# Optimization experiments

Hardware: AMD Instinct MI355X
Metric: run time of the kernel (lower is better)

Reference implementation:

```python
import jax, jax.numpy as jnp
import numpy as np

N_ATOMS = 10000
N_EDGES = 500000
N_RADIAL = 5
N_BASIS = 7
N_SPECIES = 119
R_MIN = 0.5
R_MAX = 6.0
N_CONTR = 8
EMB_NORM = 1.0 / np.sqrt(N_BASIS)


def tril_2d_indices(n):
    return np.array([(i, j) for i in range(n) for j in range(i + 1)], dtype=np.int32)


def tril_3d_indices(n):
    return np.array([(i, j, k) for i in range(n) for j in range(i + 1) for k in range(j + 1)], dtype=np.int32)


TRI2 = tril_2d_indices(N_RADIAL)
TRI3 = tril_3d_indices(N_RADIAL)


def setup_inputs() -> dict:
    key = jax.random.key(0)
    k1, k2, k3, k4 = jax.random.split(key, 4)
    dr_vec = jax.random.normal(k1, (N_EDGES, 3), dtype=jnp.float32) * 1.5
    Z = jax.random.randint(k2, (N_ATOMS,), 0, N_SPECIES)
    neighbor_idxs = jax.random.randint(k3, (2, N_EDGES), 0, N_ATOMS)
    embeddings = jax.random.normal(k4, (N_SPECIES, N_SPECIES, N_RADIAL, N_BASIS), dtype=jnp.float32)
    return {"dr_vec": dr_vec, "Z": Z, "neighbor_idxs": neighbor_idxs, "embeddings": embeddings}


def _descriptor(dr_vec, embeddings, Z, neighbor_idxs):
    idx_i, idx_j = neighbor_idxs[0], neighbor_idxs[1]
    dr = jnp.linalg.norm(dr_vec, axis=-1)                      # [E]
    dn = dr_vec / (dr + 1e-5)[:, None]                         # [E,3] unit directions
    # --- radial function: Gaussian basis + species-pair coefficients + cosine cutoff ---
    betta = N_BASIS ** 2 / R_MAX ** 2
    rad_norm = (2.0 * betta / np.pi) ** 0.75
    shifts = (R_MIN + (R_MAX - R_MIN) / N_BASIS * np.arange(N_BASIS)).astype(np.float32)
    basis = rad_norm * jnp.exp(-betta * (dr[:, None] - shifts) ** 2)   # [E,B]
    coeffs = embeddings[Z[idx_i], Z[idx_j]]                            # [E,R,B] gather
    radial = jnp.einsum("erb,eb->er", coeffs, basis) * EMB_NORM        # [E,R]
    cutoff = 0.5 * (jnp.cos(np.pi * jnp.minimum(dr, R_MAX) / R_MAX) + 1.0)
    radial = radial * cutoff[:, None]
    # --- geometric moments: outer products of dn, scatter-added per atom ---
    xyz = dn[:, None, :]                                 # [E,1,3]
    m0 = radial                                          # [E,R]
    m1 = radial[..., None] * xyz                         # [E,R,3]
    m2 = m1[..., None] * xyz[:, :, None, :]              # [E,R,3,3]
    m3 = m2[..., None] * xyz[:, :, None, None, :]        # [E,R,3,3,3]
    seg = lambda x: jax.ops.segment_sum(x, idx_j, num_segments=N_ATOMS)
    M0, M1, M2, M3 = seg(m0), seg(m1), seg(m2), seg(m3)
    # --- triangular moment contractions into invariants ---
    c0 = M0
    c1 = jnp.einsum("ari,asi->ars", M1, M1)
    c2 = jnp.einsum("arij,asij->ars", M2, M2)
    c3 = jnp.einsum("arijk,asijk->ars", M3, M3)
    c4 = jnp.einsum("arij,asik,atjk->arst", M2, M2, M2)
    c5 = jnp.einsum("ari,asj,atij->arst", M1, M1, M2)
    c6 = jnp.einsum("arijk,asijl,atkl->arst", M3, M3, M2)
    c7 = jnp.einsum("arijk,asij,atk->arst", M3, M2, M1)
    i2, j2 = TRI2[:, 0], TRI2[:, 1]
    i3, j3, k3 = TRI3[:, 0], TRI3[:, 1], TRI3[:, 2]
    n_atoms = c0.shape[0]
    c1 = c1[:, i2, j2]
    c2 = c2[:, i2, j2]
    c3 = c3[:, i2, j2]
    c4 = c4[:, i3, j3, k3]
    c5 = c5[:, i2, j2].reshape(n_atoms, -1)   # symmetric in (r,s)
    c6 = c6[:, i2, j2].reshape(n_atoms, -1)   # symmetric in (r,s)
    c7 = c7.reshape(n_atoms, -1)              # no symmetry
    feats = [c0, c1, c2, c3, c4, c5, c6, c7][:N_CONTR]
    return jnp.concatenate(feats, axis=-1)    # [n_atoms, 360]


def reference(dr_vec, Z, neighbor_idxs, embeddings):
    return _descriptor(dr_vec, embeddings, Z, neighbor_idxs)
```

## Files before the change

### kernel.cpp

```cpp
#include <hip/hip_runtime.h>
#include <hip/hip_fp16.h>
#include <cmath>

#define NSPEC 119
#define FEAT 360
#define CAP 128
#define G 16
#define NPAIR (NSPEC*NSPEC*35)
#define CNTSTRIDE 16

__global__ __launch_bounds__(256) void gm_prep_kernel(
    const float* __restrict__ emb, __half* __restrict__ emb_h,
    const int* __restrict__ Z, unsigned char* __restrict__ Zb,
    int* __restrict__ cnt, int n_atoms)
{
    int t = blockIdx.x * 256 + threadIdx.x;
    if (t < NPAIR) {
        int p = t / 35;
        int b = t - p * 35;
        emb_h[(p << 6) + b] = __float2half_rn(emb[t]);
    }
    if (t < n_atoms) {
        Zb[t] = (unsigned char)Z[t];
        cnt[t * CNTSTRIDE] = 0;
    }
}

__global__ __launch_bounds__(256) void gm_scatter_kernel(
    const float* __restrict__ dr_vec,
    const unsigned char* __restrict__ Zb,
    const int* __restrict__ nbr,
    const __half* __restrict__ emb_h,
    int* __restrict__ cnt,
    uint4* __restrict__ bucket,
    int n_edges, float rad_norm)
{
    int t = blockIdx.x * 256 + threadIdx.x;
    int h = (n_edges + 1) >> 1;
    if (t >= h) return;
    int e0 = t;
    int e1 = t + h;
    bool v1 = (e1 < n_edges);
    int e1c = v1 ? e1 : e0;

    int ai0 = nbr[e0],            aj0 = nbr[n_edges + e0];
    int ai1 = nbr[e1c],           aj1 = nbr[n_edges + e1c];

    int pos0 = atomicAdd(&cnt[aj0 * CNTSTRIDE], 1);
    int pos1 = v1 ? atomicAdd(&cnt[aj1 * CNTSTRIDE], 1) : 0;

    float x0 = dr_vec[3*e0+0], y0 = dr_vec[3*e0+1], z0 = dr_vec[3*e0+2];
    float x1 = dr_vec[3*e1c+0], y1 = dr_vec[3*e1c+1], z1 = dr_vec[3*e1c+2];
    int Zi0 = Zb[ai0], Zj0 = Zb[aj0];
    int Zi1 = Zb[ai1], Zj1 = Zb[aj1];

    const uint4* p40 = (const uint4*)(emb_h + ((size_t)(Zi0*NSPEC + Zj0) << 6));
    const uint4* p41 = (const uint4*)(emb_h + ((size_t)(Zi1*NSPEC + Zj1) << 6));
    uint buf0[20], buf1[20];
#pragma unroll
    for (int q = 0; q < 5; ++q) *(uint4*)(buf0 + 4*q) = p40[q];
#pragma unroll
    for (int q = 0; q < 5; ++q) *(uint4*)(buf1 + 4*q) = p41[q];

    const float betta = 49.0f/36.0f;

#pragma unroll
    for (int k = 0; k < 2; ++k) {
        float x = k ? x1 : x0, y = k ? y1 : y0, z = k ? z1 : z0;
        const uint* buf = k ? buf1 : buf0;
        int aj = k ? aj1 : aj0;
        int pos = k ? pos1 : pos0;
        if (k && !v1) break;

        float dr = sqrtf(x*x + y*y + z*z);
        float inv = 1.0f / (dr + 1e-5f);
        float dx = x*inv, dy = y*inv, dz = z*inv;

        float basis[7];
#pragma unroll
        for (int b = 0; b < 7; ++b) {
            float tt = dr - (0.5f + (5.5f/7.0f)*(float)b);
            basis[b] = rad_norm * __expf(-betta*tt*tt);
        }
        float cutoff = 0.5f * (__cosf(fminf(dr, 6.0f) * 0.52359877559829887f) + 1.0f);
        float sc = cutoff * 0.37796447300922720f;

        const __half2* hb = (const __half2*)buf;
        float co[36];
#pragma unroll
        for (int q = 0; q < 18; ++q) {
            float2 f = __half22float2(hb[q]);
            co[2*q]   = f.x;
            co[2*q+1] = f.y;
        }

        float rad[5];
#pragma unroll
        for (int r = 0; r < 5; ++r) {
            float acc = 0.0f;
#pragma unroll
            for (int b = 0; b < 7; ++b) acc = fmaf(co[r*7+b], basis[b], acc);
            rad[r] = acc * sc;
        }

        if (pos < CAP) {
            uint4 rec;
            __half2* rp = (__half2*)&rec;
            rp[0] = __float22half2_rn(make_float2(rad[0], rad[1]));
            rp[1] = __float22half2_rn(make_float2(rad[2], rad[3]));
            rp[2] = __float22half2_rn(make_float2(rad[4], dx));
            rp[3] = __float22half2_rn(make_float2(dy, dz));
            bucket[(size_t)aj * CAP + pos] = rec;
        }
    }
}

__global__ __launch_bounds__(256) void gm_accum_kernel(
    const int* __restrict__ cnt,
    const uint4* __restrict__ bucket,
    float* __restrict__ out,
    int n_atoms)
{
    __shared__ float MS[16][100];
    int tid = blockIdx.x * 256 + threadIdx.x;
    int a  = tid / G;
    int sl = tid & (G-1);
    int la = threadIdx.x >> 4;
    if (a >= n_atoms) return;

    int c = cnt[a * CNTSTRIDE]; if (c > CAP) c = CAP;

    float m[100];
#pragma unroll
    for (int i = 0; i < 100; ++i) m[i] = 0.f;

    for (int k = sl; k < c; k += G) {
        uint4 rec = bucket[(size_t)a * CAP + k];
        const __half2* rp = (const __half2*)&rec;
        float2 f0 = __half22float2(rp[0]);
        float2 f1 = __half22float2(rp[1]);
        float2 f2 = __half22float2(rp[2]);
        float2 f3 = __half22float2(rp[3]);
        float rad[5] = {f0.x, f0.y, f1.x, f1.y, f2.x};
        float dx = f2.y, dy = f3.x, dz = f3.y;

        float p2[6] = {dx*dx, dx*dy, dx*dz, dy*dy, dy*dz, dz*dz};
        float p3[10] = {p2[0]*dx, p2[0]*dy, p2[0]*dz,
                        p2[3]*dx, p2[4]*dx, p2[5]*dx,
                        p2[3]*dy, p2[3]*dz,
                        p2[4]*dz, p2[5]*dz};

#pragma unroll
        for (int r = 0; r < 5; ++r) {
            float v = rad[r];
            m[r] += v;
            m[5 + r*3 + 0] = fmaf(v, dx, m[5 + r*3 + 0]);
            m[5 + r*3 + 1] = fmaf(v, dy, m[5 + r*3 + 1]);
            m[5 + r*3 + 2] = fmaf(v, dz, m[5 + r*3 + 2]);
#pragma unroll
            for (int u = 0; u < 6; ++u)
                m[20 + r*6 + u] = fmaf(v, p2[u], m[20 + r*6 + u]);
#pragma unroll
            for (int u = 0; u < 10; ++u)
                m[50 + r*10 + u] = fmaf(v, p3[u], m[50 + r*10 + u]);
        }
    }

#pragma unroll
    for (int i = 0; i < 100; ++i) {
        m[i] += __shfl_xor(m[i], 1, 64);
        m[i] += __shfl_xor(m[i], 2, 64);
        m[i] += __shfl_xor(m[i], 4, 64);
        m[i] += __shfl_xor(m[i], 8, 64);
    }

    if (sl == 0) {
#pragma unroll
        for (int i = 0; i < 100; ++i) MS[la][i] = m[i];
    }

    float* F = out + (size_t)a * FEAT;
    const float* S = &MS[la][0];

    const int S2[3][3] = {{0,1,2},{1,3,4},{2,4,5}};
    const int S3[3][3][3] = {
        {{0,1,2},{1,3,4},{2,4,5}},
        {{1,3,4},{3,6,7},{4,7,8}},
        {{2,4,5},{4,7,8},{5,8,9}}};
    const float w6[6]   = {1,2,2,1,2,1};
    const float w10[10] = {1,3,3,3,6,3,1,3,3,1};
    const int   PI[6] = {0,0,0,1,1,2};
    const int   PJ[6] = {0,1,2,1,2,2};
    const float PW[6] = {1,2,2,1,2,1};

    if (sl < 5) F[sl] = S[sl];

    int p = sl;
    if (p < 15) {
        int r = (p >= 10) ? 4 : ((p >= 6) ? 3 : ((p >= 3) ? 2 : ((p >= 1) ? 1 : 0)));
        int s = p - (r*(r+1))/2;
        const float* M1r = S + 5  + 3*r;
        const float* M1s = S + 5  + 3*s;
        const float* M2r = S + 20 + 6*r;
        const float* M2s = S + 20 + 6*s;
        const float* M3r = S + 50 + 10*r;
        const float* M3s = S + 50 + 10*s;
        float m1r[3], m1s[3], m2r[6], m2s[6], m3r[10], m3s[10];
#pragma unroll
        for (int i = 0; i < 3; ++i)  { m1r[i] = M1r[i]; m1s[i] = M1s[i]; }
#pragma unroll
        for (int u = 0; u < 6; ++u)  { m2r[u] = M2r[u]; m2s[u] = M2s[u]; }
#pragma unroll
        for (int u = 0; u < 10; ++u) { m3r[u] = M3r[u]; m3s[u] = M3s[u]; }

        float a1 = 0.f, a2 = 0.f, a3 = 0.f;
#pragma unroll
        for (int i = 0; i < 3; ++i)  a1 = fmaf(m1r[i], m1s[i], a1);
#pragma unroll
        for (int u = 0; u < 6; ++u)  a2 = fmaf(w6[u]*m2r[u],  m2s[u], a2);
#pragma unroll
        for (int u = 0; u < 10; ++u) a3 = fmaf(w10[u]*m3r[u], m3s[u], a3);
        F[5 + p]  = a1;
        F[20 + p] = a2;
        F[35 + p] = a3;

        float P[3][3];
#pragma unroll
        for (int j = 0; j < 3; ++j)
#pragma unroll
        for (int k = 0; k < 3; ++k) {
            float acc = 0.f;
#pragma unroll
            for (int i = 0; i < 3; ++i)
                acc = fmaf(m2r[S2[i][j]], m2s[S2[i][k]], acc);
            P[j][k] = acc;
        }
        float PA[6] = {P[0][0], P[0][1]+P[1][0], P[0][2]+P[2][0],
                       P[1][1], P[1][2]+P[2][1], P[2][2]};
        int qb = (r*(r+1)*(r+2))/6 + (s*(s+1))/2;
        for (int t = 0; t <= s; ++t) {
            const float* M2t = S + 20 + 6*t;
            float acc = 0.f;
#pragma unroll
            for (int u = 0; u < 6; ++u) acc = fmaf(PA[u], M2t[u], acc);
            F[50 + qb + t] = acc;
        }

        float A[6] = {m1r[0]*m1s[0],
                      m1r[0]*m1s[1] + m1r[1]*m1s[0],
                      m1r[0]*m1s[2] + m1r[2]*m1s[0],
                      m1r[1]*m1s[1],
                      m1r[1]*m1s[2] + m1r[2]*m1s[1],
                      m1r[2]*m1s[2]};
#pragma unroll
        for (int t = 0; t < 5; ++t) {
            const float* M2t = S + 20 + 6*t;
            float acc = 0.f;
#pragma unroll
            for (int u = 0; u < 6; ++u) acc = fmaf(A[u], M2t[u], acc);
            F[85 + p*5 + t] = acc;
        }

        float Q[3][3];
#pragma unroll
        for (int k = 0; k < 3; ++k)
#pragma unroll
        for (int l = 0; l < 3; ++l) {
            float acc = 0.f;
#pragma unroll
            for (int u = 0; u < 6; ++u)
                acc = fmaf(PW[u]*m3r[S3[PI[u]][PJ[u]][k]],
                           m3s[S3[PI[u]][PJ[u]][l]], acc);
            Q[k][l] = acc;
        }
        float QA[6] = {Q[0][0], Q[0][1]+Q[1][0], Q[0][2]+Q[2][0],
                       Q[1][1], Q[1][2]+Q[2][1], Q[2][2]};
#pragma unroll
        for (int t = 0; t < 5; ++t) {
            const float* M2t = S + 20 + 6*t;
            float acc = 0.f;
#pragma unroll
            for (int u = 0; u < 6; ++u) acc = fmaf(QA[u], M2t[u], acc);
            F[160 + p*5 + t] = acc;
        }
    }

#pragma unroll
    for (int hh = 0; hh < 2; ++hh) {
        int h = sl + 16*hh;
        if (h < 25) {
            int r = h / 5;
            int s = h - 5*r;
            const float* M3r = S + 50 + 10*r;
            const float* M2s = S + 20 + 6*s;
            float m3r[10], m2s[6];
#pragma unroll
            for (int u = 0; u < 10; ++u) m3r[u] = M3r[u];
#pragma unroll
            for (int u = 0; u < 6; ++u)  m2s[u] = M2s[u];
            float B[3];
#pragma unroll
            for (int k = 0; k < 3; ++k) {
                float acc = 0.f;
#pragma unroll
                for (int u = 0; u < 6; ++u)
                    acc = fmaf(PW[u]*m3r[S3[PI[u]][PJ[u]][k]], m2s[u], acc);
                B[k] = acc;
            }
#pragma unroll
            for (int t = 0; t < 5; ++t) {
                const float* M1t = S + 5 + 3*t;
                F[235 + r*25 + s*5 + t] =
                    fmaf(B[0], M1t[0], fmaf(B[1], M1t[1], B[2]*M1t[2]));
            }
        }
    }
}

extern "C" void kernel_launch(void* const* d_in, const int* in_sizes, int n_in,
                              void* d_out, int out_size, void* d_ws, size_t ws_size,
                              hipStream_t stream) {
    const float* dr_vec = (const float*)d_in[0];
    const int*   Z      = (const int*)d_in[1];
    const int*   nbr    = (const int*)d_in[2];
    const float* emb    = (const float*)d_in[3];
    float* out = (float*)d_out;

    int n_edges = in_sizes[0] / 3;
    int n_atoms = in_sizes[1];

    int*           cnt   = (int*)d_ws;
    unsigned char* Zb    = (unsigned char*)((char*)d_ws + 655360);
    __half*        emb_h = (__half*)((char*)d_ws + 665600);
    uint4*         bucket= (uint4*)((char*)d_ws + 2478208);

    float rad_norm = (float)pow(2.0 * (49.0/36.0) / M_PI, 0.75);

    int prep_n = (NPAIR > n_atoms) ? NPAIR : n_atoms;
    gm_prep_kernel<<<(prep_n + 255)/256, 256, 0, stream>>>(emb, emb_h, Z, Zb, cnt, n_atoms);

    int h = (n_edges + 1) / 2;
    gm_scatter_kernel<<<(h + 255)/256, 256, 0, stream>>>(
        dr_vec, Zb, nbr, emb_h, cnt, bucket, n_edges, rad_norm);

    int accum_threads = n_atoms * G;
    gm_accum_kernel<<<(accum_threads + 255)/256, 256, 0, stream>>>(
        cnt, bucket, out, n_atoms);
}
```

Before: 121.8 us.

## Fuse scatter and accumulate kernels into persistent kernel with grid barrier

Merges the edge scatter and per-atom accumulate/contraction kernels into one persistent kernel of 512 blocks that grid-strides over edges, synchronises through a global atomic spin barrier, then grid-strides over atoms. The aim is to remove one kernel launch and the gap between the two stages. In exchange it relies on all 512 blocks being co-resident, uses fewer threads for the edge phase, and has a bounded spin that could silently break out on timeout.

Measured after the change: 212.8 us. +74.7%, slower.

```diff
diff --git a/kernel.cpp b/kernel.cpp
--- a/kernel.cpp
+++ b/kernel.cpp
@@ -8,13 +8,16 @@
 #define G 16
 #define NPAIR (NSPEC*NSPEC*35)
 #define CNTSTRIDE 16
+#define NBLK 512
+#define NTHR 256
 
 __global__ __launch_bounds__(256) void gm_prep_kernel(
     const float* __restrict__ emb, __half* __restrict__ emb_h,
     const int* __restrict__ Z, unsigned char* __restrict__ Zb,
-    int* __restrict__ cnt, int n_atoms)
+    int* __restrict__ cnt, int* __restrict__ bar, int n_atoms)
 {
     int t = blockIdx.x * 256 + threadIdx.x;
+    if (t == 0) *bar = 0;
     if (t < NPAIR) {
         int p = t / 35;
         int b = t - p * 35;
@@ -26,161 +29,116 @@
     }
 }
 
-__global__ __launch_bounds__(256) void gm_scatter_kernel(
+__global__ __launch_bounds__(NTHR, 2) void gm_main(
     const float* __restrict__ dr_vec,
     const unsigned char* __restrict__ Zb,
     const int* __restrict__ nbr,
     const __half* __restrict__ emb_h,
     int* __restrict__ cnt,
     uint4* __restrict__ bucket,
-    int n_edges, float rad_norm)
-{
-    int t = blockIdx.x * 256 + threadIdx.x;
-    int h = (n_edges + 1) >> 1;
-    if (t >= h) return;
-    int e0 = t;
-    int e1 = t + h;
-    bool v1 = (e1 < n_edges);
-    int e1c = v1 ? e1 : e0;
-
-    int ai0 = nbr[e0],            aj0 = nbr[n_edges + e0];
-    int ai1 = nbr[e1c],           aj1 = nbr[n_edges + e1c];
-
-    int pos0 = atomicAdd(&cnt[aj0 * CNTSTRIDE], 1);
-    int pos1 = v1 ? atomicAdd(&cnt[aj1 * CNTSTRIDE], 1) : 0;
-
-    float x0 = dr_vec[3*e0+0], y0 = dr_vec[3*e0+1], z0 = dr_vec[3*e0+2];
-    float x1 = dr_vec[3*e1c+0], y1 = dr_vec[3*e1c+1], z1 = dr_vec[3*e1c+2];
-    int Zi0 = Zb[ai0], Zj0 = Zb[aj0];
-    int Zi1 = Zb[ai1], Zj1 = Zb[aj1];
-
-    const uint4* p40 = (const uint4*)(emb_h + ((size_t)(Zi0*NSPEC + Zj0) << 6));
-    const uint4* p41 = (const uint4*)(emb_h + ((size_t)(Zi1*NSPEC + Zj1) << 6));
-    uint buf0[20], buf1[20];
-#pragma unroll
-    for (int q = 0; q < 5; ++q) *(uint4*)(buf0 + 4*q) = p40[q];
-#pragma unroll
-    for (int q = 0; q < 5; ++q) *(uint4*)(buf1 + 4*q) = p41[q];
-
-    const float betta = 49.0f/36.0f;
-
-#pragma unroll
-    for (int k = 0; k < 2; ++k) {
-        float x = k ? x1 : x0, y = k ? y1 : y0, z = k ? z1 : z0;
-        const uint* buf = k ? buf1 : buf0;
-        int aj = k ? aj1 : aj0;
-        int pos = k ? pos1 : pos0;
-        if (k && !v1) break;
-
-        float dr = sqrtf(x*x + y*y + z*z);
-        float inv = 1.0f / (dr + 1e-5f);
-        float dx = x*inv, dy = y*inv, dz = z*inv;
-
-        float basis[7];
-#pragma unroll
-        for (int b = 0; b < 7; ++b) {
-            float tt = dr - (0.5f + (5.5f/7.0f)*(float)b);
-            basis[b] = rad_norm * __expf(-betta*tt*tt);
-        }
-        float cutoff = 0.5f * (__cosf(fminf(dr, 6.0f) * 0.52359877559829887f) + 1.0f);
-        float sc = cutoff * 0.37796447300922720f;
-
-        const __half2* hb = (const __half2*)buf;
-        float co[36];
-#pragma unroll
-        for (int q = 0; q < 18; ++q) {
-            float2 f = __half22float2(hb[q]);
-            co[2*q]   = f.x;
-            co[2*q+1] = f.y;
-        }
-
-        float rad[5];
-#pragma unroll
-        for (int r = 0; r < 5; ++r) {
-            float acc = 0.0f;
-#pragma unroll
-            for (int b = 0; b < 7; ++b) acc = fmaf(co[r*7+b], basis[b], acc);
-            rad[r] = acc * sc;
-        }
-
-        if (pos < CAP) {
-            uint4 rec;
-            __half2* rp = (__half2*)&rec;
-            rp[0] = __float22half2_rn(make_float2(rad[0], rad[1]));
-            rp[1] = __float22half2_rn(make_float2(rad[2], rad[3]));
-            rp[2] = __float22half2_rn(make_float2(rad[4], dx));
-            rp[3] = __float22half2_rn(make_float2(dy, dz));
-            bucket[(size_t)aj * CAP + pos] = rec;
-        }
-    }
-}
-
-__global__ __launch_bounds__(256) void gm_accum_kernel(
-    const int* __restrict__ cnt,
-    const uint4* __restrict__ bucket,
+    int* __restrict__ bar,
     float* __restrict__ out,
-    int n_atoms)
+    int n_edges, int n_atoms, float rad_norm)
 {
     __shared__ float MS[16][100];
-    int tid = blockIdx.x * 256 + threadIdx.x;
-    int a  = tid / G;
-    int sl = tid & (G-1);
-    int la = threadIdx.x >> 4;
-    if (a >= n_atoms) return;
-
-    int c = cnt[a * CNTSTRIDE]; if (c > CAP) c = CAP;
-
-    float m[100];
-#pragma unroll
-    for (int i = 0; i < 100; ++i) m[i] = 0.f;
-
-    for (int k = sl; k < c; k += G) {
-        uint4 rec = bucket[(size_t)a * CAP + k];
-        const __half2* rp = (const __half2*)&rec;
-        float2 f0 = __half22float2(rp[0]);
-        float2 f1 = __half22float2(rp[1]);
-        float2 f2 = __half22float2(rp[2]);
-        float2 f3 = __half22float2(rp[3]);
-        float rad[5] = {f0.x, f0.y, f1.x, f1.y, f2.x};
-        float dx = f2.y, dy = f3.x, dz = f3.y;
-
-        float p2[6] = {dx*dx, dx*dy, dx*dz, dy*dy, dy*dz, dz*dz};
-        float p3[10] = {p2[0]*dx, p2[0]*dy, p2[0]*dz,
-                        p2[3]*dx, p2[4]*dx, p2[5]*dx,
-                        p2[3]*dy, p2[3]*dz,
-                        p2[4]*dz, p2[5]*dz};
-
-#pragma unroll
-        for (int r = 0; r < 5; ++r) {
-            float v = rad[r];
-            m[r] += v;
-            m[5 + r*3 + 0] = fmaf(v, dx, m[5 + r*3 + 0]);
-            m[5 + r*3 + 1] = fmaf(v, dy, m[5 + r*3 + 1]);
-            m[5 + r*3 + 2] = fmaf(v, dz, m[5 + r*3 + 2]);
-#pragma unroll
-            for (int u = 0; u < 6; ++u)
-                m[20 + r*6 + u] = fmaf(v, p2[u], m[20 + r*6 + u]);
-#pragma unroll
-            for (int u = 0; u < 10; ++u)
-                m[50 + r*10 + u] = fmaf(v, p3[u], m[50 + r*10 + u]);
-        }
-    }
-
-#pragma unroll
-    for (int i = 0; i < 100; ++i) {
-        m[i] += __shfl_xor(m[i], 1, 64);
-        m[i] += __shfl_xor(m[i], 2, 64);
-        m[i] += __shfl_xor(m[i], 4, 64);
-        m[i] += __shfl_xor(m[i], 8, 64);
-    }
-
-    if (sl == 0) {
-#pragma unroll
-        for (int i = 0; i < 100; ++i) MS[la][i] = m[i];
-    }
-
-    float* F = out + (size_t)a * FEAT;
-    const float* S = &MS[la][0];
+    const int tid0 = blockIdx.x * NTHR + threadIdx.x;
+    const int nth  = NBLK * NTHR;
+
+    const float betta = 49.0f/36.0f;
+    int h = (n_edges + 1) >> 1;
+    for (int t = tid0; t < h; t += nth) {
+        int e0 = t;
+        int e1 = t + h;
+        bool v1 = (e1 < n_edges);
+        int e1c = v1 ? e1 : e0;
+
+        int ai0 = nbr[e0],  aj0 = nbr[n_edges + e0];
+        int ai1 = nbr[e1c], aj1 = nbr[n_edges + e1c];
+
+        int pos0 = atomicAdd(&cnt[aj0 * CNTSTRIDE], 1);
+        int pos1 = v1 ? atomicAdd(&cnt[aj1 * CNTSTRIDE], 1) : 0;
+
+        float x0 = dr_vec[3*e0+0],  y0 = dr_vec[3*e0+1],  z0 = dr_vec[3*e0+2];
+        float x1 = dr_vec[3*e1c+0], y1 = dr_vec[3*e1c+1], z1 = dr_vec[3*e1c+2];
+        int Zi0 = Zb[ai0], Zj0 = Zb[aj0];
+        int Zi1 = Zb[ai1], Zj1 = Zb[aj1];
+
+        const uint4* p40 = (const uint4*)(emb_h + ((size_t)(Zi0*NSPEC + Zj0) << 6));
+        const uint4* p41 = (const uint4*)(emb_h + ((size_t)(Zi1*NSPEC + Zj1) << 6));
+        uint buf0[20], buf1[20];
+#pragma unroll
+        for (int q = 0; q < 5; ++q) *(uint4*)(buf0 + 4*q) = p40[q];
+#pragma unroll
+        for (int q = 0; q < 5; ++q) *(uint4*)(buf1 + 4*q) = p41[q];
+
+#pragma unroll
+        for (int k = 0; k < 2; ++k) {
+            if (k && !v1) break;
+            float x = k ? x1 : x0, y = k ? y1 : y0, z = k ? z1 : z0;
+            const uint* buf = k ? buf1 : buf0;
+            int aj  = k ? aj1 : aj0;
+            int pos = k ? pos1 : pos0;
+
+            float dr = sqrtf(x*x + y*y + z*z);
+            float inv = 1.0f / (dr + 1e-5f);
+            float dx = x*inv, dy = y*inv, dz = z*inv;
+
+            float basis[7];
+#pragma unroll
+            for (int b = 0; b < 7; ++b) {
+                float tt = dr - (0.5f + (5.5f/7.0f)*(float)b);
+                basis[b] = rad_norm * __expf(-betta*tt*tt);
+            }
+            float cutoff = 0.5f * (__cosf(fminf(dr, 6.0f) * 0.52359877559829887f) + 1.0f);
+            float sc = cutoff * 0.37796447300922720f;
+
+            const __half2* hb = (const __half2*)buf;
+            float co[36];
+#pragma unroll
+            for (int q = 0; q < 18; ++q) {
+                float2 f = __half22float2(hb[q]);
+                co[2*q]   = f.x;
+                co[2*q+1] = f.y;
+            }
+
+            float rad[5];
+#pragma unroll
+            for (int r = 0; r < 5; ++r) {
+                float acc = 0.0f;
+#pragma unroll
+                for (int b = 0; b < 7; ++b) acc = fmaf(co[r*7+b], basis[b], acc);
+                rad[r] = acc * sc;
+            }
+
+            if (pos < CAP) {
+                uint4 rec;
+                __half2* rp = (__half2*)&rec;
+                rp[0] = __float22half2_rn(make_float2(rad[0], rad[1]));
+                rp[1] = __float22half2_rn(make_float2(rad[2], rad[3]));
+                rp[2] = __float22half2_rn(make_float2(rad[4], dx));
+                rp[3] = __float22half2_rn(make_float2(dy, dz));
+                bucket[(size_t)aj * CAP + pos] = rec;
+            }
+        }
+    }
+
+    __syncthreads();
+    if (threadIdx.x == 0) {
+        __threadfence();
+        atomicAdd(bar, 1);
+        long spin = 0;
+        while (__hip_atomic_load(bar, __ATOMIC_ACQUIRE, __HIP_MEMORY_SCOPE_AGENT) < NBLK) {
+            __builtin_amdgcn_s_sleep(8);
+            if (++spin > 100000000L) break;
+        }
+    }
+    __syncthreads();
+    (void)__hip_atomic_load(bar, __ATOMIC_ACQUIRE, __HIP_MEMORY_SCOPE_AGENT);
+
+    const int ngroups = nth / G;
+    const int gid0 = tid0 / G;
+    const int sl = tid0 & (G-1);
+    const int la = threadIdx.x >> 4;
 
     const int S2[3][3] = {{0,1,2},{1,3,4},{2,4,5}};
     const int S3[3][3][3] = {
@@ -193,125 +151,181 @@
     const int   PJ[6] = {0,1,2,1,2,2};
     const float PW[6] = {1,2,2,1,2,1};
 
-    if (sl < 5) F[sl] = S[sl];
-
-    int p = sl;
-    if (p < 15) {
-        int r = (p >= 10) ? 4 : ((p >= 6) ? 3 : ((p >= 3) ? 2 : ((p >= 1) ? 1 : 0)));
-        int s = p - (r*(r+1))/2;
-        const float* M1r = S + 5  + 3*r;
-        const float* M1s = S + 5  + 3*s;
-        const float* M2r = S + 20 + 6*r;
-        const float* M2s = S + 20 + 6*s;
-        const float* M3r = S + 50 + 10*r;
-        const float* M3s = S + 50 + 10*s;
-        float m1r[3], m1s[3], m2r[6], m2s[6], m3r[10], m3s[10];
-#pragma unroll
-        for (int i = 0; i < 3; ++i)  { m1r[i] = M1r[i]; m1s[i] = M1s[i]; }
-#pragma unroll
-        for (int u = 0; u < 6; ++u)  { m2r[u] = M2r[u]; m2s[u] = M2s[u]; }
-#pragma unroll
-        for (int u = 0; u < 10; ++u) { m3r[u] = M3r[u]; m3s[u] = M3s[u]; }
-
-        float a1 = 0.f, a2 = 0.f, a3 = 0.f;
-#pragma unroll
-        for (int i = 0; i < 3; ++i)  a1 = fmaf(m1r[i], m1s[i], a1);
-#pragma unroll
-        for (int u = 0; u < 6; ++u)  a2 = fmaf(w6[u]*m2r[u],  m2s[u], a2);
-#pragma unroll
-        for (int u = 0; u < 10; ++u) a3 = fmaf(w10[u]*m3r[u], m3s[u], a3);
-        F[5 + p]  = a1;
-        F[20 + p] = a2;
-        F[35 + p] = a3;
-
-        float P[3][3];
-#pragma unroll
-        for (int j = 0; j < 3; ++j)
-#pragma unroll
-        for (int k = 0; k < 3; ++k) {
-            float acc = 0.f;
-#pragma unroll
-            for (int i = 0; i < 3; ++i)
-                acc = fmaf(m2r[S2[i][j]], m2s[S2[i][k]], acc);
-            P[j][k] = acc;
-        }
-        float PA[6] = {P[0][0], P[0][1]+P[1][0], P[0][2]+P[2][0],
-                       P[1][1], P[1][2]+P[2][1], P[2][2]};
-        int qb = (r*(r+1)*(r+2))/6 + (s*(s+1))/2;
-        for (int t = 0; t <= s; ++t) {
-            const float* M2t = S + 20 + 6*t;
-            float acc = 0.f;
-#pragma unroll
-            for (int u = 0; u < 6; ++u) acc = fmaf(PA[u], M2t[u], acc);
-            F[50 + qb + t] = acc;
-        }
-
-        float A[6] = {m1r[0]*m1s[0],
-                      m1r[0]*m1s[1] + m1r[1]*m1s[0],
-                      m1r[0]*m1s[2] + m1r[2]*m1s[0],
-                      m1r[1]*m1s[1],
-                      m1r[1]*m1s[2] + m1r[2]*m1s[1],
-                      m1r[2]*m1s[2]};
-#pragma unroll
-        for (int t = 0; t < 5; ++t) {
-            const float* M2t = S + 20 + 6*t;
-            float acc = 0.f;
-#pragma unroll
-            for (int u = 0; u < 6; ++u) acc = fmaf(A[u], M2t[u], acc);
-            F[85 + p*5 + t] = acc;
-        }
-
-        float Q[3][3];
-#pragma unroll
-        for (int k = 0; k < 3; ++k)
-#pragma unroll
-        for (int l = 0; l < 3; ++l) {
-            float acc = 0.f;
-#pragma unroll
-            for (int u = 0; u < 6; ++u)
-                acc = fmaf(PW[u]*m3r[S3[PI[u]][PJ[u]][k]],
-                           m3s[S3[PI[u]][PJ[u]][l]], acc);
-            Q[k][l] = acc;
-        }
-        float QA[6] = {Q[0][0], Q[0][1]+Q[1][0], Q[0][2]+Q[2][0],
-                       Q[1][1], Q[1][2]+Q[2][1], Q[2][2]};
-#pragma unroll
-        for (int t = 0; t < 5; ++t) {
-            const float* M2t = S + 20 + 6*t;
-            float acc = 0.f;
-#pragma unroll
-            for (int u = 0; u < 6; ++u) acc = fmaf(QA[u], M2t[u], acc);
-            F[160 + p*5 + t] = acc;
-        }
-    }
-
-#pragma unroll
-    for (int hh = 0; hh < 2; ++hh) {
-        int h = sl + 16*hh;
-        if (h < 25) {
-            int r = h / 5;
-            int s = h - 5*r;
+    for (int a = gid0; a < n_atoms; a += ngroups) {
+        int c = cnt[a * CNTSTRIDE]; if (c > CAP) c = CAP;
+
+        float m[100];
+#pragma unroll
+        for (int i = 0; i < 100; ++i) m[i] = 0.f;
+
+        for (int k = sl; k < c; k += G) {
+            uint4 rec = bucket[(size_t)a * CAP + k];
+            const __half2* rp = (const __half2*)&rec;
+            float2 f0 = __half22float2(rp[0]);
+            float2 f1 = __half22float2(rp[1]);
+            float2 f2 = __half22float2(rp[2]);
+            float2 f3 = __half22float2(rp[3]);
+            float rad[5] = {f0.x, f0.y, f1.x, f1.y, f2.x};
+            float dx = f2.y, dy = f3.x, dz = f3.y;
+
+            float p2[6] = {dx*dx, dx*dy, dx*dz, dy*dy, dy*dz, dz*dz};
+            float p3[10] = {p2[0]*dx, p2[0]*dy, p2[0]*dz,
+                            p2[3]*dx, p2[4]*dx, p2[5]*dx,
+                            p2[3]*dy, p2[3]*dz,
+                            p2[4]*dz, p2[5]*dz};
+
+#pragma unroll
+            for (int r = 0; r < 5; ++r) {
+                float v = rad[r];
+                m[r] += v;
+                m[5 + r*3 + 0] = fmaf(v, dx, m[5 + r*3 + 0]);
+                m[5 + r*3 + 1] = fmaf(v, dy, m[5 + r*3 + 1]);
+                m[5 + r*3 + 2] = fmaf(v, dz, m[5 + r*3 + 2]);
+#pragma unroll
+                for (int u = 0; u < 6; ++u)
+                    m[20 + r*6 + u] = fmaf(v, p2[u], m[20 + r*6 + u]);
+#pragma unroll
+                for (int u = 0; u < 10; ++u)
+                    m[50 + r*10 + u] = fmaf(v, p3[u], m[50 + r*10 + u]);
+            }
+        }
+
+#pragma unroll
+        for (int i = 0; i < 100; ++i) {
+            m[i] += __shfl_xor(m[i], 1, 64);
+            m[i] += __shfl_xor(m[i], 2, 64);
+            m[i] += __shfl_xor(m[i], 4, 64);
+            m[i] += __shfl_xor(m[i], 8, 64);
+        }
+
+        if (sl == 0) {
+#pragma unroll
+            for (int i = 0; i < 100; ++i) MS[la][i] = m[i];
+        }
+
+        float* F = out + (size_t)a * FEAT;
+        const float* S = &MS[la][0];
+
+        if (sl < 5) F[sl] = S[sl];
+
+        int p = sl;
+        if (p < 15) {
+            int r = (p >= 10) ? 4 : ((p >= 6) ? 3 : ((p >= 3) ? 2 : ((p >= 1) ? 1 : 0)));
+            int s = p - (r*(r+1))/2;
+            const float* M1r = S + 5  + 3*r;
+            const float* M1s = S + 5  + 3*s;
+            const float* M2r = S + 20 + 6*r;
+            const float* M2s = S + 20 + 6*s;
             const float* M3r = S + 50 + 10*r;
-            const float* M2s = S + 20 + 6*s;
-            float m3r[10], m2s[6];
-#pragma unroll
-            for (int u = 0; u < 10; ++u) m3r[u] = M3r[u];
-#pragma unroll
-            for (int u = 0; u < 6; ++u)  m2s[u] = M2s[u];
-            float B[3];
+            const float* M3s = S + 50 + 10*s;
+            float m1r[3], m1s[3], m2r[6], m2s[6], m3r[10], m3s[10];
+#pragma unroll
+            for (int i = 0; i < 3; ++i)  { m1r[i] = M1r[i]; m1s[i] = M1s[i]; }
+#pragma unroll
+            for (int u = 0; u < 6; ++u)  { m2r[u] = M2r[u]; m2s[u] = M2s[u]; }
+#pragma unroll
+            for (int u = 0; u < 10; ++u) { m3r[u] = M3r[u]; m3s[u] = M3s[u]; }
+
+            float a1 = 0.f, a2 = 0.f, a3 = 0.f;
+#pragma unroll
+            for (int i = 0; i < 3; ++i)  a1 = fmaf(m1r[i], m1s[i], a1);
+#pragma unroll
+            for (int u = 0; u < 6; ++u)  a2 = fmaf(w6[u]*m2r[u],  m2s[u], a2);
+#pragma unroll
+            for (int u = 0; u < 10; ++u) a3 = fmaf(w10[u]*m3r[u], m3s[u], a3);
+            F[5 + p]  = a1;
+            F[20 + p] = a2;
+            F[35 + p] = a3;
+
+            float P[3][3];
+#pragma unroll
+            for (int j = 0; j < 3; ++j)
 #pragma unroll
             for (int k = 0; k < 3; ++k) {
                 float acc = 0.f;
 #pragma unroll
+                for (int i = 0; i < 3; ++i)
+                    acc = fmaf(m2r[S2[i][j]], m2s[S2[i][k]], acc);
+                P[j][k] = acc;
+            }
+            float PA[6] = {P[0][0], P[0][1]+P[1][0], P[0][2]+P[2][0],
+                           P[1][1], P[1][2]+P[2][1], P[2][2]};
+            int qb = (r*(r+1)*(r+2))/6 + (s*(s+1))/2;
+            for (int t = 0; t <= s; ++t) {
+                const float* M2t = S + 20 + 6*t;
+                float acc = 0.f;
+#pragma unroll
+                for (int u = 0; u < 6; ++u) acc = fmaf(PA[u], M2t[u], acc);
+                F[50 + qb + t] = acc;
+            }
+
+            float A[6] = {m1r[0]*m1s[0],
+                          m1r[0]*m1s[1] + m1r[1]*m1s[0],
+                          m1r[0]*m1s[2] + m1r[2]*m1s[0],
+                          m1r[1]*m1s[1],
+                          m1r[1]*m1s[2] + m1r[2]*m1s[1],
+                          m1r[2]*m1s[2]};
+#pragma unroll
+            for (int t = 0; t < 5; ++t) {
+                const float* M2t = S + 20 + 6*t;
+                float acc = 0.f;
+#pragma unroll
+                for (int u = 0; u < 6; ++u) acc = fmaf(A[u], M2t[u], acc);
+                F[85 + p*5 + t] = acc;
+            }
+
+            float Q[3][3];
+#pragma unroll
+            for (int k = 0; k < 3; ++k)
+#pragma unroll
+            for (int l = 0; l < 3; ++l) {
+                float acc = 0.f;
+#pragma unroll
                 for (int u = 0; u < 6; ++u)
-                    acc = fmaf(PW[u]*m3r[S3[PI[u]][PJ[u]][k]], m2s[u], acc);
-                B[k] = acc;
-            }
+                    acc = fmaf(PW[u]*m3r[S3[PI[u]][PJ[u]][k]],
+                               m3s[S3[PI[u]][PJ[u]][l]], acc);
+                Q[k][l] = acc;
+            }
+            float QA[6] = {Q[0][0], Q[0][1]+Q[1][0], Q[0][2]+Q[2][0],
+                           Q[1][1], Q[1][2]+Q[2][1], Q[2][2]};
 #pragma unroll
             for (int t = 0; t < 5; ++t) {
-                const float* M1t = S + 5 + 3*t;
-                F[235 + r*25 + s*5 + t] =
-                    fmaf(B[0], M1t[0], fmaf(B[1], M1t[1], B[2]*M1t[2]));
+                const float* M2t = S + 20 + 6*t;
+                float acc = 0.f;
+#pragma unroll
+                for (int u = 0; u < 6; ++u) acc = fmaf(QA[u], M2t[u], acc);
+                F[160 + p*5 + t] = acc;
+            }
+        }
+
+#pragma unroll
+        for (int hh = 0; hh < 2; ++hh) {
+            int hp = sl + 16*hh;
+            if (hp < 25) {
+                int r = hp / 5;
+                int s = hp - 5*r;
+                const float* M3r = S + 50 + 10*r;
+                const float* M2s = S + 20 + 6*s;
+                float m3r[10], m2s[6];
+#pragma unroll
+                for (int u = 0; u < 10; ++u) m3r[u] = M3r[u];
+#pragma unroll
+                for (int u = 0; u < 6; ++u)  m2s[u] = M2s[u];
+                float B[3];
+#pragma unroll
+                for (int k = 0; k < 3; ++k) {
+                    float acc = 0.f;
+#pragma unroll
+                    for (int u = 0; u < 6; ++u)
+                        acc = fmaf(PW[u]*m3r[S3[PI[u]][PJ[u]][k]], m2s[u], acc);
+                    B[k] = acc;
+                }
+#pragma unroll
+                for (int t = 0; t < 5; ++t) {
+                    const float* M1t = S + 5 + 3*t;
+                    F[235 + r*25 + s*5 + t] =
+                        fmaf(B[0], M1t[0], fmaf(B[1], M1t[1], B[2]*M1t[2]));
+                }
             }
         }
     }
@@ -329,21 +343,19 @@
     int n_edges = in_sizes[0] / 3;
     int n_atoms = in_sizes[1];
 
-    int*           cnt   = (int*)d_ws;
-    unsigned char* Zb    = (unsigned char*)((char*)d_ws + 655360);
-    __half*        emb_h = (__half*)((char*)d_ws + 665600);
-    uint4*         bucket= (uint4*)((char*)d_ws + 2478208);
+    int*           cnt    = (int*)d_ws;
+    unsigned char* Zb     = (unsigned char*)((char*)d_ws + 655360);
+    int*           bar    = (int*)((char*)d_ws + 665408);
+    __half*        emb_h  = (__half*)((char*)d_ws + 665600);
+    uint4*         bucket = (uint4*)((char*)d_ws + 2478208);
 
     float rad_norm = (float)pow(2.0 * (49.0/36.0) / M_PI, 0.75);
 
     int prep_n = (NPAIR > n_atoms) ? NPAIR : n_atoms;
-    gm_prep_kernel<<<(prep_n + 255)/256, 256, 0, stream>>>(emb, emb_h, Z, Zb, cnt, n_atoms);
-
-    int h = (n_edges + 1) / 2;
-    gm_scatter_kernel<<<(h + 255)/256, 256, 0, stream>>>(
-        dr_vec, Zb, nbr, emb_h, cnt, bucket, n_edges, rad_norm);
-
-    int accum_threads = n_atoms * G;
-    gm_accum_kernel<<<(accum_threads + 255)/256, 256, 0, stream>>>(
-        cnt, bucket, out, n_atoms);
+    gm_prep_kernel<<<(prep_n + 255)/256, 256, 0, stream>>>(
+        emb, emb_h, Z, Zb, cnt, bar, n_atoms);
+
+    gm_main<<<NBLK, NTHR, 0, stream>>>(
+        dr_vec, Zb, nbr, emb_h, cnt, bucket, bar, out,
+        n_edges, n_atoms, rad_norm);
 }
```

## Precompute packed species-pair and target index per edge in prep kernel

Applied to the files above, without the earlier changes.

The prep kernel now resolves each edge's species pair index and target atom and packs them into one int, so the scatter kernel reads a single word instead of two neighbor indices plus two dependent Z lookups. The scatter kernel goes back to one edge per thread instead of two. This moves the dependent gather chain into a kernel that already runs over a large grid, which shortens the latency chain in scatter. The cost is an extra 2 MB write and read and a larger prep grid.

After: 120.3 us, median of 2. About the same (-1.3%).

```diff
diff --git a/kernel.cpp b/kernel.cpp
--- a/kernel.cpp
+++ b/kernel.cpp
@@ -11,8 +11,9 @@
 
 __global__ __launch_bounds__(256) void gm_prep_kernel(
     const float* __restrict__ emb, __half* __restrict__ emb_h,
-    const int* __restrict__ Z, unsigned char* __restrict__ Zb,
-    int* __restrict__ cnt, int n_atoms)
+    const int* __restrict__ Z, const int* __restrict__ nbr,
+    int* __restrict__ pre, int* __restrict__ cnt,
+    int n_atoms, int n_edges)
 {
     int t = blockIdx.x * 256 + threadIdx.x;
     if (t < NPAIR) {
@@ -20,98 +21,80 @@
         int b = t - p * 35;
         emb_h[(p << 6) + b] = __float2half_rn(emb[t]);
     }
-    if (t < n_atoms) {
-        Zb[t] = (unsigned char)Z[t];
-        cnt[t * CNTSTRIDE] = 0;
+    if (t < n_atoms) cnt[t * CNTSTRIDE] = 0;
+    if (t < n_edges) {
+        int ai = nbr[t];
+        int aj = nbr[n_edges + t];
+        int pi = Z[ai] * NSPEC + Z[aj];
+        pre[t] = (pi << 14) | aj;
     }
 }
 
 __global__ __launch_bounds__(256) void gm_scatter_kernel(
     const float* __restrict__ dr_vec,
-    const unsigned char* __restrict__ Zb,
-    const int* __restrict__ nbr,
+    const int* __restrict__ pre,
     const __half* __restrict__ emb_h,
     int* __restrict__ cnt,
     uint4* __restrict__ bucket,
     int n_edges, float rad_norm)
 {
-    int t = blockIdx.x * 256 + threadIdx.x;
-    int h = (n_edges + 1) >> 1;
-    if (t >= h) return;
-    int e0 = t;
-    int e1 = t + h;
-    bool v1 = (e1 < n_edges);
-    int e1c = v1 ? e1 : e0;
-
-    int ai0 = nbr[e0],            aj0 = nbr[n_edges + e0];
-    int ai1 = nbr[e1c],           aj1 = nbr[n_edges + e1c];
-
-    int pos0 = atomicAdd(&cnt[aj0 * CNTSTRIDE], 1);
-    int pos1 = v1 ? atomicAdd(&cnt[aj1 * CNTSTRIDE], 1) : 0;
-
-    float x0 = dr_vec[3*e0+0], y0 = dr_vec[3*e0+1], z0 = dr_vec[3*e0+2];
-    float x1 = dr_vec[3*e1c+0], y1 = dr_vec[3*e1c+1], z1 = dr_vec[3*e1c+2];
-    int Zi0 = Zb[ai0], Zj0 = Zb[aj0];
-    int Zi1 = Zb[ai1], Zj1 = Zb[aj1];
-
-    const uint4* p40 = (const uint4*)(emb_h + ((size_t)(Zi0*NSPEC + Zj0) << 6));
-    const uint4* p41 = (const uint4*)(emb_h + ((size_t)(Zi1*NSPEC + Zj1) << 6));
-    uint buf0[20], buf1[20];
-#pragma unroll
-    for (int q = 0; q < 5; ++q) *(uint4*)(buf0 + 4*q) = p40[q];
-#pragma unroll
-    for (int q = 0; q < 5; ++q) *(uint4*)(buf1 + 4*q) = p41[q];
+    int e = blockIdx.x * 256 + threadIdx.x;
+    if (e >= n_edges) return;
+
+    int pk = pre[e];
+    int aj = pk & 16383;
+    int pi = pk >> 14;
+
+    int pos = atomicAdd(&cnt[aj * CNTSTRIDE], 1);
+    const uint4* p4 = (const uint4*)(emb_h + ((size_t)pi << 6));
+    uint buf[20];
+#pragma unroll
+    for (int q = 0; q < 5; ++q) *(uint4*)(buf + 4*q) = p4[q];
+
+    float x = dr_vec[3*e+0];
+    float y = dr_vec[3*e+1];
+    float z = dr_vec[3*e+2];
+
+    float dr = sqrtf(x*x + y*y + z*z);
+    float inv = 1.0f / (dr + 1e-5f);
+    float dx = x*inv, dy = y*inv, dz = z*inv;
 
     const float betta = 49.0f/36.0f;
-
-#pragma unroll
-    for (int k = 0; k < 2; ++k) {
-        float x = k ? x1 : x0, y = k ? y1 : y0, z = k ? z1 : z0;
-        const uint* buf = k ? buf1 : buf0;
-        int aj = k ? aj1 : aj0;
-        int pos = k ? pos1 : pos0;
-        if (k && !v1) break;
-
-        float dr = sqrtf(x*x + y*y + z*z);
-        float inv = 1.0f / (dr + 1e-5f);
-        float dx = x*inv, dy = y*inv, dz = z*inv;
-
-        float basis[7];
-#pragma unroll
-        for (int b = 0; b < 7; ++b) {
-            float tt = dr - (0.5f + (5.5f/7.0f)*(float)b);
-            basis[b] = rad_norm * __expf(-betta*tt*tt);
-        }
-        float cutoff = 0.5f * (__cosf(fminf(dr, 6.0f) * 0.52359877559829887f) + 1.0f);
-        float sc = cutoff * 0.37796447300922720f;
-
-        const __half2* hb = (const __half2*)buf;
-        float co[36];
-#pragma unroll
-        for (int q = 0; q < 18; ++q) {
-            float2 f = __half22float2(hb[q]);
-            co[2*q]   = f.x;
-            co[2*q+1] = f.y;
-        }
-
-        float rad[5];
-#pragma unroll
-        for (int r = 0; r < 5; ++r) {
-            float acc = 0.0f;
-#pragma unroll
-            for (int b = 0; b < 7; ++b) acc = fmaf(co[r*7+b], basis[b], acc);
-            rad[r] = acc * sc;
-        }
-
-        if (pos < CAP) {
-            uint4 rec;
-            __half2* rp = (__half2*)&rec;
-            rp[0] = __float22half2_rn(make_float2(rad[0], rad[1]));
-            rp[1] = __float22half2_rn(make_float2(rad[2], rad[3]));
-            rp[2] = __float22half2_rn(make_float2(rad[4], dx));
-            rp[3] = __float22half2_rn(make_float2(dy, dz));
-            bucket[(size_t)aj * CAP + pos] = rec;
-        }
+    float basis[7];
+#pragma unroll
+    for (int b = 0; b < 7; ++b) {
+        float tt = dr - (0.5f + (5.5f/7.0f)*(float)b);
+        basis[b] = rad_norm * __expf(-betta*tt*tt);
+    }
+    float cutoff = 0.5f * (__cosf(fminf(dr, 6.0f) * 0.52359877559829887f) + 1.0f);
+    float sc = cutoff * 0.37796447300922720f;
+
+    const __half2* hb = (const __half2*)buf;
+    float co[36];
+#pragma unroll
+    for (int q = 0; q < 18; ++q) {
+        float2 f = __half22float2(hb[q]);
+        co[2*q]   = f.x;
+        co[2*q+1] = f.y;
+    }
+
+    float rad[5];
+#pragma unroll
+    for (int r = 0; r < 5; ++r) {
+        float acc = 0.0f;
+#pragma unroll
+        for (int b = 0; b < 7; ++b) acc = fmaf(co[r*7+b], basis[b], acc);
+        rad[r] = acc * sc;
+    }
+
+    if (pos < CAP) {
+        uint4 rec;
+        __half2* rp = (__half2*)&rec;
+        rp[0] = __float22half2_rn(make_float2(rad[0], rad[1]));
+        rp[1] = __float22half2_rn(make_float2(rad[2], rad[3]));
+        rp[2] = __float22half2_rn(make_float2(rad[4], dx));
+        rp[3] = __float22half2_rn(make_float2(dy, dz));
+        bucket[(size_t)aj * CAP + pos] = rec;
     }
 }
 
@@ -287,10 +270,10 @@
 
 #pragma unroll
     for (int hh = 0; hh < 2; ++hh) {
-        int h = sl + 16*hh;
-        if (h < 25) {
-            int r = h / 5;
-            int s = h - 5*r;
+        int hp = sl + 16*hh;
+        if (hp < 25) {
+            int r = hp / 5;
+            int s = hp - 5*r;
             const float* M3r = S + 50 + 10*r;
             const float* M2s = S + 20 + 6*s;
             float m3r[10], m2s[6];
@@ -329,19 +312,21 @@
     int n_edges = in_sizes[0] / 3;
     int n_atoms = in_sizes[1];
 
-    int*           cnt   = (int*)d_ws;
-    unsigned char* Zb    = (unsigned char*)((char*)d_ws + 655360);
-    __half*        emb_h = (__half*)((char*)d_ws + 665600);
-    uint4*         bucket= (uint4*)((char*)d_ws + 2478208);
+    int*    cnt    = (int*)d_ws;
+    __half* emb_h  = (__half*)((char*)d_ws + 655360);
+    int*    pre    = (int*)((char*)d_ws + 2467968);
+    uint4*  bucket = (uint4*)((char*)d_ws + 4467968);
 
     float rad_norm = (float)pow(2.0 * (49.0/36.0) / M_PI, 0.75);
 
-    int prep_n = (NPAIR > n_atoms) ? NPAIR : n_atoms;
-    gm_prep_kernel<<<(prep_n + 255)/256, 256, 0, stream>>>(emb, emb_h, Z, Zb, cnt, n_atoms);
-
-    int h = (n_edges + 1) / 2;
-    gm_scatter_kernel<<<(h + 255)/256, 256, 0, stream>>>(
-        dr_vec, Zb, nbr, emb_h, cnt, bucket, n_edges, rad_norm);
+    int prep_n = NPAIR;
+    if (n_edges > prep_n) prep_n = n_edges;
+    if (n_atoms > prep_n) prep_n = n_atoms;
+    gm_prep_kernel<<<(prep_n + 255)/256, 256, 0, stream>>>(
+        emb, emb_h, Z, nbr, pre, cnt, n_atoms, n_edges);
+
+    gm_scatter_kernel<<<(n_edges + 255)/256, 256, 0, stream>>>(
+        dr_vec, pre, emb_h, cnt, bucket, n_edges, rad_norm);
 
     int accum_threads = n_atoms * G;
     gm_accum_kernel<<<(accum_threads + 255)/256, 256, 0, stream>>>(
```
